# Performance work log

Hardware: AMD Instinct MI355X
Metric: run time of the kernel (lower is better)

## Reference

```python
import jax, jax.numpy as jnp
import numpy as np

B, S, HID = 16, 1024, 768
H, DH = 12, HID // 12


def setup_inputs() -> dict:
    key = jax.random.key(0)
    ks = jax.random.split(key, 10)
    scale = 1.0 / np.sqrt(HID)
    return {
        "hidden_states": jax.random.normal(ks[0], (B, S, HID), jnp.float32),
        "Wq": jax.random.normal(ks[1], (HID, HID), jnp.float32) * scale,
        "bq": jnp.zeros((HID,), jnp.float32),
        "Wk": jax.random.normal(ks[2], (HID, HID), jnp.float32) * scale,
        "bk": jnp.zeros((HID,), jnp.float32),
        "Wv": jax.random.normal(ks[3], (HID, HID), jnp.float32) * scale,
        "bv": jnp.zeros((HID,), jnp.float32),
        # torch init is zeros; use small randn so the linear-attention correction term is exercised
        "phi_k": jax.random.normal(ks[4], (1, H, DH, 1), jnp.float32) * 0.02,
        "phi_kv": jax.random.normal(ks[5], (1, H, DH, DH), jnp.float32) * 0.02,
    }


def _heads(x):
    # [B,S,HID] -> [B,H,S,DH]
    return x.reshape(B, S, H, DH).transpose(0, 2, 1, 3)


def reference(hidden_states, Wq, bq, Wk, bk, Wv, bv, phi_k, phi_kv):
    q = _heads(hidden_states @ Wq.T + bq)
    k = _heads(hidden_states @ Wk.T + bk)
    v = _heads(hidden_states @ Wv.T + bv)

    # phi(x) = ELU(x / d^0.25) + 1   (dropout disabled: eval-mode reference)
    phi_q = jax.nn.elu(q / jnp.asarray(DH, jnp.float32) ** 0.25) + 1.0

    # full softmax-style attention scores with max-subtract
    A = jnp.einsum("bhsd,bhtd->bhst", q, k) / jnp.sqrt(jnp.asarray(DH, jnp.float32))
    max_A = jnp.max(A, axis=-1, keepdims=True)          # [B,H,S,1]
    exp_max_A = jnp.exp(max_A)
    A = jnp.exp(A - max_A)                              # [B,H,S,S]

    # custom normalizer: softmax mass + linear-attention correction
    D = jnp.sum(A, axis=-1, keepdims=True) + jnp.matmul(phi_q, jnp.abs(phi_k)) / exp_max_A

    ctx = (jnp.matmul(A, v) + jnp.matmul(phi_q, phi_kv) / exp_max_A) / D  # [B,H,S,DH]
    out = ctx.transpose(0, 2, 1, 3).reshape(B, S, HID)
    return out
```

## Files before the change

kernel.cpp:

```cpp
#include <hip/hip_runtime.h>
#include <cstdint>
#include <cstddef>

typedef _Float16 f16x8 __attribute__((ext_vector_type(8)));
typedef _Float16 f16x4 __attribute__((ext_vector_type(4)));
typedef float    f32x4 __attribute__((ext_vector_type(4)));
typedef unsigned u32;
typedef const u32 __attribute__((address_space(1)))* gas_ptr;
typedef u32 __attribute__((address_space(3)))* las_ptr;

#define MFMA16(a, b, c) __builtin_amdgcn_mfma_f32_16x16x32_f16((a), (b), (c), 0, 0, 0)

static constexpr int Bb   = 16;
static constexpr int Ss   = 1024;
static constexpr int HID  = 768;
static constexpr int Hh   = 12;
static constexpr int DH   = 64;
static constexpr int Mrows = Bb * Ss;
static constexpr int N3    = 3 * HID;

static constexpr float QSCL  = 0.125f * 1.44269504088896f;
static constexpr float PHSCL = 1.9605161f;

__global__ void prep(const float* __restrict__ hs, _Float16* __restrict__ A16,
                     const float* __restrict__ Wq, const float* __restrict__ Wk,
                     const float* __restrict__ Wv, const float* __restrict__ bq,
                     const float* __restrict__ bk, const float* __restrict__ bv,
                     _Float16* __restrict__ Wt, float* __restrict__ bias) {
    const int i = blockIdx.x * 256 + threadIdx.x;
    if (i < Mrows * HID / 4) {
        float4 v = ((const float4*)hs)[i];
        f16x4 o;
        o[0] = (_Float16)v.x; o[1] = (_Float16)v.y;
        o[2] = (_Float16)v.z; o[3] = (_Float16)v.w;
        ((f16x4*)A16)[i] = o;
    }
    if (i < N3 * HID / 8) {
        const int i8 = i * 8;
        int n = i8 / HID;
        int k = i8 - n * HID;
        int sel = n / HID;
        int nn  = n - sel * HID;
        const float* W = (sel == 0) ? Wq : (sel == 1) ? Wk : Wv;
        const float* wp = W + (size_t)nn * HID + k;
        float4 v0 = *(const float4*)wp;
        float4 v1 = *(const float4*)(wp + 4);
        uint4 o;
        o.x = __builtin_bit_cast(u32, __builtin_amdgcn_cvt_pkrtz(v0.x, v0.y));
        o.y = __builtin_bit_cast(u32, __builtin_amdgcn_cvt_pkrtz(v0.z, v0.w));
        o.z = __builtin_bit_cast(u32, __builtin_amdgcn_cvt_pkrtz(v1.x, v1.y));
        o.w = __builtin_bit_cast(u32, __builtin_amdgcn_cvt_pkrtz(v1.z, v1.w));
        *(uint4*)(Wt + i8) = o;
    }
    if (i < N3) {
        int wsel = i / HID, j = i - wsel * HID;
        bias[i] = (wsel == 0) ? bq[j] : (wsel == 1) ? bk[j] : bv[j];
    }
}

__global__ __launch_bounds__(256, 2) void qkv_gemm(
    const _Float16* __restrict__ A, const _Float16* __restrict__ Bt,
    const float* __restrict__ bias,
    _Float16* __restrict__ Qo, _Float16* __restrict__ Ko, _Float16* __restrict__ VTo) {
    __shared__ _Float16 As[128 * 64];
    __shared__ _Float16 Bs[128 * 64];
    const int tid  = threadIdx.x;
    const int lane = tid & 63, wid = tid >> 6;
    const int g = lane >> 4, c = lane & 15;
    const int bm = blockIdx.x & 127, bn = blockIdx.x >> 7;
    const int m0 = bm * 128, n0 = bn * 128;
    const int wm = wid >> 1, wn = wid & 1;

    const int srk = ((lane & 7) ^ (lane >> 3)) << 3;

    f32x4 acc[4][4] = {};

    for (int kt = 0; kt < HID; kt += 64) {
        if (kt) __syncthreads();
#pragma unroll
        for (int i = 0; i < 4; ++i) {
            const int ch  = i * 256 + wid * 64 + lane;
            const int row = ch >> 3;
            __builtin_amdgcn_global_load_lds(
                (gas_ptr)(A + (size_t)(m0 + row) * HID + kt + srk),
                (las_ptr)(As + (i * 256 + wid * 64) * 8), 16, 0, 0);
            __builtin_amdgcn_global_load_lds(
                (gas_ptr)(Bt + (size_t)(n0 + row) * HID + kt + srk),
                (las_ptr)(Bs + (i * 256 + wid * 64) * 8), 16, 0, 0);
        }
        __syncthreads();

#pragma unroll
        for (int kk = 0; kk < 2; ++kk) {
            f16x8 af[4], bf[4];
#pragma unroll
            for (int mi = 0; mi < 4; ++mi) {
                const int row = wm * 64 + mi * 16 + c;
                af[mi] = *(const f16x8*)((const char*)As + row * 128 + ((((kk * 4 + g) ^ (c & 7))) << 4));
            }
#pragma unroll
            for (int ni = 0; ni < 4; ++ni) {
                const int row = wn * 64 + ni * 16 + c;
                bf[ni] = *(const f16x8*)((const char*)Bs + row * 128 + ((((kk * 4 + g) ^ (c & 7))) << 4));
            }
#pragma unroll
            for (int mi = 0; mi < 4; ++mi)
#pragma unroll
                for (int ni = 0; ni < 4; ++ni)
                    acc[mi][ni] = MFMA16(af[mi], bf[ni], acc[mi][ni]);
        }
    }

#pragma unroll
    for (int ni = 0; ni < 4; ++ni) {
        const int col    = n0 + wn * 64 + ni * 16 + c;
        const int which  = col / HID;
        const int within = col - which * HID;
        const int hh = within >> 6, d = within & 63;
        const float bias_v = bias[col];
        const float scl = (which == 0) ? QSCL : 1.0f;
#pragma unroll
        for (int mi = 0; mi < 4; ++mi) {
            const int rowg0 = m0 + wm * 64 + mi * 16 + g * 4;
            const int bidx = rowg0 >> 10, s0 = rowg0 & 1023;
            const int bh   = bidx * Hh + hh;
            f16x4 hv4;
#pragma unroll
            for (int r = 0; r < 4; ++r)
                hv4[r] = (_Float16)((acc[mi][ni][r] + bias_v) * scl);
            if (which == 2) {
                const int base64 = (m0 + wm * 64) & 1023;
                const int p = 32 * (mi >> 1) + 8 * g + 4 * (mi & 1);
                *(uint2*)(VTo + ((size_t)bh * DH + d) * Ss + base64 + p) = __builtin_bit_cast(uint2, hv4);
            } else if (which == 0) {
#pragma unroll
                for (int r = 0; r < 4; ++r)
                    Qo[((size_t)bh * Ss + s0 + r) * DH + d] = hv4[r];
            } else {
#pragma unroll
                for (int r = 0; r < 4; ++r)
                    Ko[((size_t)bh * Ss + s0 + r) * DH + d] = hv4[r];
            }
        }
    }
}

__global__ __launch_bounds__(256) void attn_kernel(
    const _Float16* __restrict__ Q, const _Float16* __restrict__ K,
    const _Float16* __restrict__ VT, const float* __restrict__ phi_k,
    const float* __restrict__ phi_kv, float* __restrict__ out) {
    __shared__ _Float16 Kb[2][64 * 64];
    __shared__ _Float16 Vb[2][64 * 64];

    const int tid  = threadIdx.x;
    const int lane = tid & 63, w = tid >> 6;
    const int g = lane >> 4, c = lane & 15;

    const int wg = (blockIdx.x & 7) * 192 + (blockIdx.x >> 3);
    const int bh = wg >> 3, qt = wg & 7;
    const int b = bh / Hh, h = bh - b * Hh;
    const size_t base = (size_t)bh * Ss * DH;
    const _Float16* Kg = K + base;
    const _Float16* Vg = VT + base;

    const int srow = lane >> 3;
    const int scol = (((lane & 7) ^ srow) << 4) >> 1;
    const int sw = (c & 7) << 4;

    const _Float16* Qp = Q + base + (size_t)(qt * 128 + w * 32 + c) * DH + g * 8;
    f16x8 aq[2][2];
    aq[0][0] = *(const f16x8*)(Qp);
    aq[0][1] = *(const f16x8*)(Qp + 32);
    aq[1][0] = *(const f16x8*)(Qp + 16 * DH);
    aq[1][1] = *(const f16x8*)(Qp + 16 * DH + 32);

    float part[2] = {0.f, 0.f};
    f32x4 acco[2][4] = {};

    auto stage = [&](int bf, int t0) {
#pragma unroll
        for (int i = 0; i < 2; ++i) {
            const int row0 = w * 16 + i * 8;
            __builtin_amdgcn_global_load_lds(
                (gas_ptr)(Kg + (size_t)(t0 + row0 + srow) * DH + scol),
                (las_ptr)(&Kb[bf][row0 * 64]), 16, 0, 0);
            __builtin_amdgcn_global_load_lds(
                (gas_ptr)(Vg + (size_t)(row0 + srow) * Ss + t0 + scol),
                (las_ptr)(&Vb[bf][row0 * 64]), 16, 0, 0);
        }
    };

    stage(0, 0);
    __syncthreads();

    for (int t0 = 0; t0 < Ss; t0 += 64) {
        const int bf = (t0 >> 6) & 1;
        if (t0 + 64 < Ss) stage(bf ^ 1, t0 + 64);

        f32x4 z[2][4];
        __builtin_amdgcn_s_setprio(1);
#pragma unroll
        for (int nt = 0; nt < 4; ++nt) {
            const char* kb = (const char*)&Kb[bf][0] + (nt * 16 + c) * 128;
            f16x8 bk0 = *(const f16x8*)(kb + ((g * 16) ^ sw));
            f16x8 bk1 = *(const f16x8*)(kb + ((64 + g * 16) ^ sw));
            f32x4 z0 = {}, z1 = {};
            z0 = MFMA16(bk0, aq[0][0], z0);
            z0 = MFMA16(bk1, aq[0][1], z0);
            z1 = MFMA16(bk0, aq[1][0], z1);
            z1 = MFMA16(bk1, aq[1][1], z1);
            z[0][nt] = z0;
            z[1][nt] = z1;
        }
        __builtin_amdgcn_s_setprio(0);

        f16x8 pb[2][2];
#pragma unroll
        for (int mb = 0; mb < 2; ++mb) {
#pragma unroll
            for (int kk = 0; kk < 2; ++kk) {
                float e0 = __builtin_amdgcn_exp2f(z[mb][2 * kk][0]);
                float e1 = __builtin_amdgcn_exp2f(z[mb][2 * kk][1]);
                float e2 = __builtin_amdgcn_exp2f(z[mb][2 * kk][2]);
                float e3 = __builtin_amdgcn_exp2f(z[mb][2 * kk][3]);
                float e4 = __builtin_amdgcn_exp2f(z[mb][2 * kk + 1][0]);
                float e5 = __builtin_amdgcn_exp2f(z[mb][2 * kk + 1][1]);
                float e6 = __builtin_amdgcn_exp2f(z[mb][2 * kk + 1][2]);
                float e7 = __builtin_amdgcn_exp2f(z[mb][2 * kk + 1][3]);
                part[mb] += (e0 + e1 + e2 + e3) + (e4 + e5 + e6 + e7);
                uint4 pk;
                pk.x = __builtin_bit_cast(u32, __builtin_amdgcn_cvt_pkrtz(e0, e1));
                pk.y = __builtin_bit_cast(u32, __builtin_amdgcn_cvt_pkrtz(e2, e3));
                pk.z = __builtin_bit_cast(u32, __builtin_amdgcn_cvt_pkrtz(e4, e5));
                pk.w = __builtin_bit_cast(u32, __builtin_amdgcn_cvt_pkrtz(e6, e7));
                pb[mb][kk] = __builtin_bit_cast(f16x8, pk);
            }
        }

        __builtin_amdgcn_s_setprio(1);
#pragma unroll
        for (int nd = 0; nd < 4; ++nd) {
            const char* vb = (const char*)&Vb[bf][0] + (nd * 16 + c) * 128;
#pragma unroll
            for (int kk = 0; kk < 2; ++kk) {
                f16x8 va = *(const f16x8*)(vb + ((kk * 64 + g * 16) ^ sw));
                acco[0][nd] = MFMA16(va, pb[0][kk], acco[0][nd]);
                acco[1][nd] = MFMA16(va, pb[1][kk], acco[1][nd]);
            }
        }
        __builtin_amdgcn_s_setprio(0);
        __syncthreads();
    }

    const float* phk = phi_k + h * DH;
    const float* pkv = phi_kv + h * DH * DH;

    f16x8 pq2[2][2];
    float invD[2];
#pragma unroll
    for (int mb = 0; mb < 2; ++mb) {
        const _Float16* Qr = Q + base + (size_t)(qt * 128 + w * 32 + mb * 16 + c) * DH;
        float dot = 0.f;
#pragma unroll
        for (int kk = 0; kk < 2; ++kk) {
            f16x4 qa = *(const f16x4*)(Qr + kk * 32 + 4 * g);
            f16x4 qb = *(const f16x4*)(Qr + kk * 32 + 16 + 4 * g);
            float4 fka = *(const float4*)(phk + kk * 32 + 4 * g);
            float4 fkb = *(const float4*)(phk + kk * 32 + 16 + 4 * g);
            const float fa[4] = {fka.x, fka.y, fka.z, fka.w};
            const float fb[4] = {fkb.x, fkb.y, fkb.z, fkb.w};
            f16x8 pq;
#pragma unroll
            for (int j = 0; j < 4; ++j) {
                float x0 = (float)qa[j] * PHSCL;
                float x1 = (float)qb[j] * PHSCL;
                float p0 = (x0 > 0.f) ? (x0 + 1.f) : __expf(x0);
                float p1 = (x1 > 0.f) ? (x1 + 1.f) : __expf(x1);
                dot += p0 * fabsf(fa[j]) + p1 * fabsf(fb[j]);
                pq[j]     = (_Float16)p0;
                pq[4 + j] = (_Float16)p1;
            }
            pq2[mb][kk] = pq;
        }
        dot += __shfl_xor(dot, 16);
        dot += __shfl_xor(dot, 32);
        float s = part[mb];
        s += __shfl_xor(s, 16);
        s += __shfl_xor(s, 32);
        invD[mb] = 1.f / (s + dot);
    }

#pragma unroll
    for (int nd = 0; nd < 4; ++nd) {
        f16x8 fa[2];
#pragma unroll
        for (int kk = 0; kk < 2; ++kk) {
            f16x8 t;
#pragma unroll
            for (int j = 0; j < 8; ++j) {
                int dh = kk * 32 + 16 * (j >> 2) + 4 * g + (j & 3);
                t[j] = (_Float16)pkv[dh * DH + nd * 16 + c];
            }
            fa[kk] = t;
        }
#pragma unroll
        for (int mb = 0; mb < 2; ++mb) {
            f32x4 cc = {};
            cc = MFMA16(fa[0], pq2[mb][0], cc);
            cc = MFMA16(fa[1], pq2[mb][1], cc);
            f32x4 o = (acco[mb][nd] + cc) * invD[mb];
            const int srow_o = qt * 128 + w * 32 + mb * 16 + c;
            float* op = out + ((size_t)b * Ss + srow_o) * HID + h * DH + nd * 16 + 4 * g;
            *(f32x4*)op = o;
        }
    }
}

extern "C" void kernel_launch(void* const* d_in, const int* in_sizes, int n_in,
                              void* d_out, int out_size, void* d_ws, size_t ws_size,
                              hipStream_t stream) {
    (void)in_sizes; (void)n_in; (void)out_size;
    const float* hs   = (const float*)d_in[0];
    const float* Wq   = (const float*)d_in[1];
    const float* bq   = (const float*)d_in[2];
    const float* Wk   = (const float*)d_in[3];
    const float* bk   = (const float*)d_in[4];
    const float* Wv   = (const float*)d_in[5];
    const float* bv   = (const float*)d_in[6];
    const float* phik = (const float*)d_in[7];
    const float* phikv= (const float*)d_in[8];
    float* out = (float*)d_out;

    char* ws = (char*)d_ws;
    constexpr size_t szA   = (size_t)Mrows * HID * 2;
    constexpr size_t szWt  = (size_t)N3 * HID * 2;
    constexpr size_t szBia = (size_t)N3 * 4;
    constexpr size_t szQ   = (size_t)Bb * Hh * Ss * DH * 2;
    _Float16* A16  = (_Float16*)(ws);
    _Float16* Wt   = (_Float16*)(ws + szA);
    float*    bias = (float*)(ws + szA + szWt);
    _Float16* Qb   = (_Float16*)(ws + szA + szWt + szBia);
    _Float16* Kb   = (_Float16*)(ws + szA + szWt + szBia + szQ);
    _Float16* VTb  = (_Float16*)(ws + szA + szWt + szBia + 2 * szQ);
    (void)ws_size;

    prep<<<(Mrows * HID / 4 + 255) / 256, 256, 0, stream>>>(hs, A16, Wq, Wk, Wv, bq, bk, bv, Wt, bias);
    qkv_gemm<<<dim3((Mrows / 128) * (N3 / 128)), 256, 0, stream>>>(A16, Wt, bias, Qb, Kb, VTb);
    attn_kernel<<<dim3(Bb * Hh * (Ss / 128)), 256, 0, stream>>>(Qb, Kb, VTb, phik, phikv, out);
}
```

Baseline: 174.4 us.

## Load K and V tiles directly from global memory, dropping LDS staging

Removes the double-buffered LDS staging of K and V tiles via global_load_lds and the per-iteration barrier. Each wave now reads its K and V fragments straight from global memory, relying on L1/L2 caching, since all four waves read the same tiles. This removes LDS traffic and synchronisation, but every wave re-fetches the same data from cache and loses the software prefetch overlap.

```diff
diff --git a/kernel.cpp b/kernel.cpp
--- a/kernel.cpp
+++ b/kernel.cpp
@@ -149,9 +149,6 @@
     const _Float16* __restrict__ Q, const _Float16* __restrict__ K,
     const _Float16* __restrict__ VT, const float* __restrict__ phi_k,
     const float* __restrict__ phi_kv, float* __restrict__ out) {
-    __shared__ _Float16 Kb[2][64 * 64];
-    __shared__ _Float16 Vb[2][64 * 64];
-
     const int tid  = threadIdx.x;
     const int lane = tid & 63, w = tid >> 6;
     const int g = lane >> 4, c = lane & 15;
@@ -160,12 +157,9 @@
     const int bh = wg >> 3, qt = wg & 7;
     const int b = bh / Hh, h = bh - b * Hh;
     const size_t base = (size_t)bh * Ss * DH;
-    const _Float16* Kg = K + base;
-    const _Float16* Vg = VT + base;
-
-    const int srow = lane >> 3;
-    const int scol = (((lane & 7) ^ srow) << 4) >> 1;
-    const int sw = (c & 7) << 4;
+
+    const _Float16* Kf = K + base + (size_t)c * DH + g * 8;
+    const _Float16* Vf = VT + base + (size_t)c * Ss + g * 8;
 
     const _Float16* Qp = Q + base + (size_t)(qt * 128 + w * 32 + c) * DH + g * 8;
     f16x8 aq[2][2];
@@ -177,33 +171,14 @@
     float part[2] = {0.f, 0.f};
     f32x4 acco[2][4] = {};
 
-    auto stage = [&](int bf, int t0) {
-#pragma unroll
-        for (int i = 0; i < 2; ++i) {
-            const int row0 = w * 16 + i * 8;
-            __builtin_amdgcn_global_load_lds(
-                (gas_ptr)(Kg + (size_t)(t0 + row0 + srow) * DH + scol),
-                (las_ptr)(&Kb[bf][row0 * 64]), 16, 0, 0);
-            __builtin_amdgcn_global_load_lds(
-                (gas_ptr)(Vg + (size_t)(row0 + srow) * Ss + t0 + scol),
-                (las_ptr)(&Vb[bf][row0 * 64]), 16, 0, 0);
-        }
-    };
-
-    stage(0, 0);
-    __syncthreads();
-
     for (int t0 = 0; t0 < Ss; t0 += 64) {
-        const int bf = (t0 >> 6) & 1;
-        if (t0 + 64 < Ss) stage(bf ^ 1, t0 + 64);
-
         f32x4 z[2][4];
         __builtin_amdgcn_s_setprio(1);
 #pragma unroll
         for (int nt = 0; nt < 4; ++nt) {
-            const char* kb = (const char*)&Kb[bf][0] + (nt * 16 + c) * 128;
-            f16x8 bk0 = *(const f16x8*)(kb + ((g * 16) ^ sw));
-            f16x8 bk1 = *(const f16x8*)(kb + ((64 + g * 16) ^ sw));
+            const _Float16* kp = Kf + (size_t)(t0 + nt * 16) * DH;
+            f16x8 bk0 = *(const f16x8*)(kp);
+            f16x8 bk1 = *(const f16x8*)(kp + 32);
             f32x4 z0 = {}, z1 = {};
             z0 = MFMA16(bk0, aq[0][0], z0);
             z0 = MFMA16(bk1, aq[0][1], z0);
@@ -240,16 +215,15 @@
         __builtin_amdgcn_s_setprio(1);
 #pragma unroll
         for (int nd = 0; nd < 4; ++nd) {
-            const char* vb = (const char*)&Vb[bf][0] + (nd * 16 + c) * 128;
+            const _Float16* vp = Vf + (size_t)(nd * 16) * Ss + t0;
 #pragma unroll
             for (int kk = 0; kk < 2; ++kk) {
-                f16x8 va = *(const f16x8*)(vb + ((kk * 64 + g * 16) ^ sw));
+                f16x8 va = *(const f16x8*)(vp + kk * 32);
                 acco[0][nd] = MFMA16(va, pb[0][kk], acco[0][nd]);
                 acco[1][nd] = MFMA16(va, pb[1][kk], acco[1][nd]);
             }
         }
         __builtin_amdgcn_s_setprio(0);
-        __syncthreads();
     }
 
     const float* phk = phi_k + h * DH;
```

Result: slower. 285.8 us (+63.9%).

## Software-pipeline QK of the next tile with exp and PV of the previous tile

Applied to the files above, without the earlier changes.

Restructures the attention inner loop so that the QK^T MFMAs for tile t are issued alongside the exp2, pack and PV MFMAs for tile t-1. Two score register sets alternate between the halves of a manually unrolled loop. V moves to a triple-buffered LDS ring while K stays double-buffered, so the V tile is still resident when its PV runs a step later. The aim is to hide exp and transcendental latency behind matrix-core work within each wave. In exchange it adds a second score accumulator set, which raises register pressure and could lower occupancy, and it uses more LDS.

```diff
diff --git a/kernel.cpp b/kernel.cpp
--- a/kernel.cpp
+++ b/kernel.cpp
@@ -150,7 +150,7 @@
     const _Float16* __restrict__ VT, const float* __restrict__ phi_k,
     const float* __restrict__ phi_kv, float* __restrict__ out) {
     __shared__ _Float16 Kb[2][64 * 64];
-    __shared__ _Float16 Vb[2][64 * 64];
+    __shared__ _Float16 Vb[3][64 * 64];
 
     const int tid  = threadIdx.x;
     const int lane = tid & 63, w = tid >> 6;
@@ -176,32 +176,30 @@
 
     float part[2] = {0.f, 0.f};
     f32x4 acco[2][4] = {};
-
-    auto stage = [&](int bf, int t0) {
+    f32x4 zA[2][4], zB[2][4];
+
+    auto stage = [&](int t) {
+        const int t0 = t * 64;
+        _Float16* kd = &Kb[t & 1][0];
+        _Float16* vd = &Vb[t % 3][0];
 #pragma unroll
         for (int i = 0; i < 2; ++i) {
             const int row0 = w * 16 + i * 8;
             __builtin_amdgcn_global_load_lds(
                 (gas_ptr)(Kg + (size_t)(t0 + row0 + srow) * DH + scol),
-                (las_ptr)(&Kb[bf][row0 * 64]), 16, 0, 0);
+                (las_ptr)(kd + row0 * 64), 16, 0, 0);
             __builtin_amdgcn_global_load_lds(
                 (gas_ptr)(Vg + (size_t)(row0 + srow) * Ss + t0 + scol),
-                (las_ptr)(&Vb[bf][row0 * 64]), 16, 0, 0);
+                (las_ptr)(vd + row0 * 64), 16, 0, 0);
         }
     };
 
-    stage(0, 0);
-    __syncthreads();
-
-    for (int t0 = 0; t0 < Ss; t0 += 64) {
-        const int bf = (t0 >> 6) & 1;
-        if (t0 + 64 < Ss) stage(bf ^ 1, t0 + 64);
-
-        f32x4 z[2][4];
+    auto qk_phase = [&](int t, f32x4 (&zc)[2][4]) {
+        const char* kb0 = (const char*)&Kb[t & 1][0];
         __builtin_amdgcn_s_setprio(1);
 #pragma unroll
         for (int nt = 0; nt < 4; ++nt) {
-            const char* kb = (const char*)&Kb[bf][0] + (nt * 16 + c) * 128;
+            const char* kb = kb0 + (nt * 16 + c) * 128;
             f16x8 bk0 = *(const f16x8*)(kb + ((g * 16) ^ sw));
             f16x8 bk1 = *(const f16x8*)(kb + ((64 + g * 16) ^ sw));
             f32x4 z0 = {}, z1 = {};
@@ -209,38 +207,40 @@
             z0 = MFMA16(bk1, aq[0][1], z0);
             z1 = MFMA16(bk0, aq[1][0], z1);
             z1 = MFMA16(bk1, aq[1][1], z1);
-            z[0][nt] = z0;
-            z[1][nt] = z1;
+            zc[0][nt] = z0;
+            zc[1][nt] = z1;
         }
         __builtin_amdgcn_s_setprio(0);
-
+    };
+
+    auto exppv_phase = [&](int tp, f32x4 (&zp)[2][4]) {
         f16x8 pb[2][2];
 #pragma unroll
-        for (int mb = 0; mb < 2; ++mb) {
+        for (int j = 0; j < 2; ++j) {
 #pragma unroll
             for (int kk = 0; kk < 2; ++kk) {
-                float e0 = __builtin_amdgcn_exp2f(z[mb][2 * kk][0]);
-                float e1 = __builtin_amdgcn_exp2f(z[mb][2 * kk][1]);
-                float e2 = __builtin_amdgcn_exp2f(z[mb][2 * kk][2]);
-                float e3 = __builtin_amdgcn_exp2f(z[mb][2 * kk][3]);
-                float e4 = __builtin_amdgcn_exp2f(z[mb][2 * kk + 1][0]);
-                float e5 = __builtin_amdgcn_exp2f(z[mb][2 * kk + 1][1]);
-                float e6 = __builtin_amdgcn_exp2f(z[mb][2 * kk + 1][2]);
-                float e7 = __builtin_amdgcn_exp2f(z[mb][2 * kk + 1][3]);
-                part[mb] += (e0 + e1 + e2 + e3) + (e4 + e5 + e6 + e7);
+                float e0 = __builtin_amdgcn_exp2f(zp[j][2 * kk][0]);
+                float e1 = __builtin_amdgcn_exp2f(zp[j][2 * kk][1]);
+                float e2 = __builtin_amdgcn_exp2f(zp[j][2 * kk][2]);
+                float e3 = __builtin_amdgcn_exp2f(zp[j][2 * kk][3]);
+                float e4 = __builtin_amdgcn_exp2f(zp[j][2 * kk + 1][0]);
+                float e5 = __builtin_amdgcn_exp2f(zp[j][2 * kk + 1][1]);
+                float e6 = __builtin_amdgcn_exp2f(zp[j][2 * kk + 1][2]);
+                float e7 = __builtin_amdgcn_exp2f(zp[j][2 * kk + 1][3]);
+                part[j] += (e0 + e1 + e2 + e3) + (e4 + e5 + e6 + e7);
                 uint4 pk;
                 pk.x = __builtin_bit_cast(u32, __builtin_amdgcn_cvt_pkrtz(e0, e1));
                 pk.y = __builtin_bit_cast(u32, __builtin_amdgcn_cvt_pkrtz(e2, e3));
                 pk.z = __builtin_bit_cast(u32, __builtin_amdgcn_cvt_pkrtz(e4, e5));
                 pk.w = __builtin_bit_cast(u32, __builtin_amdgcn_cvt_pkrtz(e6, e7));
-                pb[mb][kk] = __builtin_bit_cast(f16x8, pk);
-            }
-        }
-
+                pb[j][kk] = __builtin_bit_cast(f16x8, pk);
+            }
+        }
         __builtin_amdgcn_s_setprio(1);
+        const char* vb0 = (const char*)&Vb[tp % 3][0];
 #pragma unroll
         for (int nd = 0; nd < 4; ++nd) {
-            const char* vb = (const char*)&Vb[bf][0] + (nd * 16 + c) * 128;
+            const char* vb = vb0 + (nd * 16 + c) * 128;
 #pragma unroll
             for (int kk = 0; kk < 2; ++kk) {
                 f16x8 va = *(const f16x8*)(vb + ((kk * 64 + g * 16) ^ sw));
@@ -249,8 +249,27 @@
             }
         }
         __builtin_amdgcn_s_setprio(0);
+    };
+
+    stage(0);
+    stage(1);
+    __syncthreads();
+    qk_phase(0, zA);
+    __syncthreads();
+
+    for (int t = 1; t < 16; t += 2) {
+        if (t + 1 < 16) stage(t + 1);
+        qk_phase(t, zB);
+        exppv_phase(t - 1, zA);
         __syncthreads();
-    }
+        if (t + 1 < 16) {
+            if (t + 2 < 16) stage(t + 2);
+            qk_phase(t + 1, zA);
+            exppv_phase(t, zB);
+            __syncthreads();
+        }
+    }
+    exppv_phase(15, zB);
 
     const float* phk = phi_k + h * DH;
     const float* pkv = phi_kv + h * DH * DH;
```

After: 171.3 us. About the same (-1.8%).
